# Performance work log

Hardware: AMD Instinct MI355X
Metric: run time of the kernel (lower is better)

## Reference

```python
import math
import jax
import jax.numpy as jnp
import numpy as np

B = 4096        # number of contexts / segments
T = 262144      # total objects across all segments (avg 64 per segment)
F = 128         # object_size
H = 256         # hidden_size
C = 512         # context_size


def setup_inputs() -> dict:
    key = jax.random.key(0)
    ks = jax.random.split(key, 8)
    objects = jax.random.normal(ks[0], (T, F), dtype=jnp.float32)
    context = jax.random.normal(ks[1], (B, C), dtype=jnp.float32)
    # sorted segment ids; guarantee every segment non-empty by seeding one id per segment
    extra = jax.random.randint(ks[2], (T - B,), 0, B)
    segment_ids = jnp.sort(jnp.concatenate([jnp.arange(B, dtype=extra.dtype), extra])).astype(jnp.int32)
    s = 0.05
    return {
        "objects": objects,
        "context": context,
        "segment_ids": segment_ids,
        "W1": jax.random.normal(ks[3], (F, H), dtype=jnp.float32) * s,
        "b1": jnp.zeros((H,), dtype=jnp.float32),
        "W2": jax.random.normal(ks[4], (H, H), dtype=jnp.float32) * s,
        "b2": jnp.zeros((H,), dtype=jnp.float32),
        "W3": jax.random.normal(ks[5], (H, 2 * H), dtype=jnp.float32) * s,
        "b3": jnp.zeros((2 * H,), dtype=jnp.float32),
        "Wq": jax.random.normal(ks[6], (C, H), dtype=jnp.float32) * s,
        "bq": jnp.zeros((H,), dtype=jnp.float32),
    }


def reference(objects, context, segment_ids, W1, b1, W2, b2, W3, b3, Wq, bq):
    num_segments = context.shape[0]
    # kv MLP: Linear -> ReLU -> Linear -> ReLU -> Linear(2H)
    h = jax.nn.relu(objects @ W1 + b1)
    h = jax.nn.relu(h @ W2 + b2)
    kv = h @ W3 + b3                                   # [T, 2H]
    k, v = jnp.split(kv, 2, axis=1)                    # [T, H] each
    # query per object via repeat_interleave == gather by segment id
    q = (context @ Wq + bq)[segment_ids]               # [T, H]
    logits = jnp.sum(q * k, axis=1) / math.sqrt(k.shape[1])   # [T]
    # per-segment stable softmax
    m = jax.ops.segment_max(logits, segment_ids, num_segments=num_segments)
    e = jnp.exp(logits - m[segment_ids])
    z = jax.ops.segment_sum(e, segment_ids, num_segments=num_segments)
    w = e / z[segment_ids]                             # [T]
    # per-segment weighted sum of values
    embedding = jax.ops.segment_sum(w[:, None] * v, segment_ids, num_segments=num_segments)  # [B, H]
    return embedding, w
```

## Files before the change

### kernel.cpp

```cpp
#include <hip/hip_runtime.h>
#include <hip/hip_bf16.h>

#define T_TOTAL 262144
#define B_SEG   4096

typedef __attribute__((ext_vector_type(8))) short short8;
typedef __attribute__((ext_vector_type(4))) float f32x4;

__device__ __forceinline__ short f2bf(float x) {
    __hip_bfloat16 h = __float2bfloat16(x);
    return *reinterpret_cast<short*>(&h);
}
__device__ __forceinline__ float bf2f(short s) {
    unsigned u = ((unsigned)(unsigned short)s) << 16;
    return __uint_as_float(u);
}

__global__ __launch_bounds__(256) void prep_all(
    const float* __restrict__ W1, const float* __restrict__ W2,
    const float* __restrict__ W3, const float* __restrict__ Wq,
    const float* __restrict__ bq, const float* __restrict__ b3,
    const float* __restrict__ ctx, const int* __restrict__ seg,
    short* __restrict__ W1T, short* __restrict__ W2T, short* __restrict__ W3vT,
    float* __restrict__ bz, float* __restrict__ wc, float* __restrict__ c0,
    float* __restrict__ Wqz, float* __restrict__ cbuf,
    int* __restrict__ starts) {
    __shared__ __align__(16) char smem[33280];
    const int b = blockIdx.x, tid = threadIdx.x;

    if (b < 40) {
        float (*t)[68] = reinterpret_cast<float(*)[68]>(smem);
        const float* src; short* dst;
        int k0, n0_src, n0_dst, sstride, dstride;
        if (b < 8) {
            int kt = b >> 2, nt = b & 3;
            src = W1; dst = W1T; sstride = 256; dstride = 128;
            k0 = kt * 64; n0_src = nt * 64; n0_dst = nt * 64;
        } else if (b < 24) {
            int id = b - 8, kt = id >> 2, nt = id & 3;
            src = W2; dst = W2T; sstride = 256; dstride = 256;
            k0 = kt * 64; n0_src = nt * 64; n0_dst = nt * 64;
        } else {
            int id = b - 24, kt = id >> 2, nt = id & 3;
            src = W3; dst = W3vT; sstride = 512; dstride = 256;
            k0 = kt * 64; n0_src = 256 + nt * 64; n0_dst = nt * 64;
        }
        {
            int r = tid >> 4, c4 = (tid & 15) * 4;
#pragma unroll
            for (int p = 0; p < 4; p++) {
                int k = p * 16 + r;
                float4 v = *reinterpret_cast<const float4*>(
                    &src[(size_t)(k0 + k) * sstride + n0_src + c4]);
                *reinterpret_cast<float4*>(&t[k][c4]) = v;
            }
        }
        __syncthreads();
        {
            int n = tid >> 2, kq = tid & 3;
            short8 s0, s1;
#pragma unroll
            for (int i = 0; i < 8; i++) s0[i] = f2bf(t[kq * 16 + i][n]);
#pragma unroll
            for (int i = 0; i < 8; i++) s1[i] = f2bf(t[kq * 16 + 8 + i][n]);
            short* o = &dst[(size_t)(n0_dst + n) * dstride + k0 + kq * 16];
            *reinterpret_cast<short8*>(o) = s0;
            *reinterpret_cast<short8*>(o + 8) = s1;
        }
    } else if (b < 42) {
        if (b == 40) {
            float s = 0.f;
            for (int n = 0; n < 256; n += 4) {
                float4 a = *reinterpret_cast<const float4*>(&W3[(size_t)tid * 512 + n]);
                float4 v = *reinterpret_cast<const float4*>(&bq[n]);
                s += a.x * v.x + a.y * v.y + a.z * v.z + a.w * v.w;
            }
            bz[tid] = s;
        } else {
#pragma unroll
            for (int h = 0; h < 2; h++) {
                int c = h * 256 + tid;
                float s = 0.f;
                for (int n = 0; n < 256; n += 4) {
                    float4 a = *reinterpret_cast<const float4*>(&Wq[(size_t)c * 256 + n]);
                    float4 v = *reinterpret_cast<const float4*>(&b3[n]);
                    s += a.x * v.x + a.y * v.y + a.z * v.z + a.w * v.w;
                }
                wc[c] = s;
            }
            if (tid == 0) {
                float s = 0.f;
                for (int n = 0; n < 256; n++) s += bq[n] * b3[n];
                c0[0] = s;
            }
        }
    } else if (b < 554) {
        float (*wq)[260] = reinterpret_cast<float(*)[260]>(smem);
        float (*w3)[260] = reinterpret_cast<float(*)[260]>(smem + 16640);
        const int id = b - 42;
        const int c0r = (id >> 4) * 16, j0 = (id & 15) * 16;
        {
            int r = tid >> 4, nq = tid & 15;
#pragma unroll
            for (int p = 0; p < 4; p++) {
                int col = nq * 4 + p * 64;
                *reinterpret_cast<float4*>(&wq[r][col]) =
                    *reinterpret_cast<const float4*>(&Wq[(size_t)(c0r + r) * 256 + col]);
                *reinterpret_cast<float4*>(&w3[r][col]) =
                    *reinterpret_cast<const float4*>(&W3[(size_t)(j0 + r) * 512 + col]);
            }
        }
        __syncthreads();
        const int ci = tid >> 4, ji = tid & 15;
        float s = 0.f;
        for (int n = 0; n < 256; n += 4) {
            float4 a = *reinterpret_cast<const float4*>(&wq[ci][n]);
            float4 v = *reinterpret_cast<const float4*>(&w3[ji][n]);
            s += a.x * v.x + a.y * v.y + a.z * v.z + a.w * v.w;
        }
        Wqz[(size_t)(c0r + ci) * 256 + j0 + ji] = s;
    } else if (b < 682) {
        const int id = b - 554;
        const int row = id * 32 + (tid >> 3);
        const int l = tid & 7;
        float s = 0.f;
        for (int i = 0; i < 64; i += 4) {
            float4 a = *reinterpret_cast<const float4*>(&ctx[(size_t)row * 512 + l * 64 + i]);
            float4 v = *reinterpret_cast<const float4*>(&wc[l * 64 + i]);
            s += a.x * v.x + a.y * v.y + a.z * v.z + a.w * v.w;
        }
        s += __shfl_xor(s, 1); s += __shfl_xor(s, 2); s += __shfl_xor(s, 4);
        if (l == 0) cbuf[row] = s + c0[0];
    } else {
        int t = (b - 682) * 256 + tid;
        if (t < T_TOTAL) {
            int s = seg[t];
            if (t == 0) {
                for (int q = 0; q <= s; q++) starts[q] = 0;
            } else {
                int p = seg[t - 1];
                for (int q = p + 1; q <= s; q++) starts[q] = t;
            }
        }
    }
}

__global__ __launch_bounds__(256) void zq_kernel(
    const float* __restrict__ ctx, const float* __restrict__ Wqz,
    const float* __restrict__ bz, float* __restrict__ zq) {
    __shared__ float As[2][16][44];
    const int tid = threadIdx.x;
    const int tm = tid & 7, tn = tid >> 3;
    const int row0 = blockIdx.x * 32, col0 = blockIdx.y * 64;
    const int lr = tid >> 3, lk = tid & 7;

    float acc[4][2];
#pragma unroll
    for (int i = 0; i < 4; i++) { acc[i][0] = 0.f; acc[i][1] = 0.f; }

    float2 av = *reinterpret_cast<const float2*>(&ctx[(size_t)(row0 + lr) * 512 + lk * 2]);
    for (int c = 0; c < 32; c++) {
        int cur = c & 1;
        As[cur][lk * 2 + 0][lr] = av.x;
        As[cur][lk * 2 + 1][lr] = av.y;
        __syncthreads();
        if (c < 31)
            av = *reinterpret_cast<const float2*>(
                &ctx[(size_t)(row0 + lr) * 512 + (c + 1) * 16 + lk * 2]);
#pragma unroll
        for (int k = 0; k < 16; k++) {
            float4 a = *reinterpret_cast<const float4*>(&As[cur][k][tm * 4]);
            float2 b = *reinterpret_cast<const float2*>(
                &Wqz[(size_t)(c * 16 + k) * 256 + col0 + tn * 2]);
            acc[0][0] += a.x * b.x; acc[0][1] += a.x * b.y;
            acc[1][0] += a.y * b.x; acc[1][1] += a.y * b.y;
            acc[2][0] += a.z * b.x; acc[2][1] += a.z * b.y;
            acc[3][0] += a.w * b.x; acc[3][1] += a.w * b.y;
        }
    }
    float2 bv = *reinterpret_cast<const float2*>(&bz[col0 + tn * 2]);
#pragma unroll
    for (int i = 0; i < 4; i++) {
        float2 o = {acc[i][0] + bv.x, acc[i][1] + bv.y};
        *reinterpret_cast<float2*>(
            &zq[(size_t)(row0 + tm * 4 + i) * 256 + col0 + tn * 2]) = o;
    }
}

template <int K>
__device__ __forceinline__ void run_layer(
    const short* __restrict__ act, const short* __restrict__ Wt,
    int nbase, int l16, int quad, f32x4 acc[8][4]) {
    constexpr int KK = K / 32;
    const f32x4 zero = {0.f, 0.f, 0.f, 0.f};
#pragma unroll
    for (int i = 0; i < 8; i++)
#pragma unroll
        for (int j = 0; j < 4; j++) acc[i][j] = zero;

    int woff[4];
#pragma unroll
    for (int ns = 0; ns < 4; ns++)
        woff[ns] = ((nbase + ns * 16 + l16) * K + quad * 8) * 2;
    const int abase = l16 * K * 2;
    const char* actc = reinterpret_cast<const char*>(act);
    const char* wtc  = reinterpret_cast<const char*>(Wt);

    short8 wbuf[2][4];
    short8 areg[8];

#pragma unroll
    for (int ns = 0; ns < 4; ns++)
        wbuf[0][ns] = *reinterpret_cast<const short8*>(wtc + woff[ns]);

#pragma unroll
    for (int kk = 0; kk < KK; kk++) {
        if (kk + 1 < KK) {
#pragma unroll
            for (int ns = 0; ns < 4; ns++)
                wbuf[(kk + 1) & 1][ns] = *reinterpret_cast<const short8*>(
                    wtc + woff[ns] + (kk + 1) * 64);
        }
        {
            const int sg = (((kk * 4 + quad) ^ l16) * 16);
#pragma unroll
            for (int ms = 0; ms < 8; ms++)
                areg[ms] = *reinterpret_cast<const short8*>(
                    actc + abase + ms * 16 * K * 2 + sg);
        }
        const int cb = kk & 1;
#pragma unroll
        for (int ms = 0; ms < 8; ms++)
#pragma unroll
            for (int ns = 0; ns < 4; ns++)
                acc[ms][ns] = __builtin_amdgcn_mfma_f32_16x16x32_bf16(
                    wbuf[cb][ns], areg[ms], acc[ms][ns], 0, 0, 0);
    }
}

__global__ __launch_bounds__(256, 2) void mlp_kernel(
    const float* __restrict__ objects, const int* __restrict__ seg_ids,
    const short* __restrict__ W1T, const short* __restrict__ W2T,
    const short* __restrict__ W3vT,
    const float* __restrict__ b1, const float* __restrict__ b2,
    const float* __restrict__ b3,
    const float* __restrict__ zqbuf, const float* __restrict__ cbuf,
    float* __restrict__ logits_out, short* __restrict__ vout) {
    __shared__ __align__(16) short bufH[128 * 256];
    __shared__ float slots[4][128];

    const int tid  = threadIdx.x;
    const int wave = tid >> 6;
    const int lane = tid & 63;
    const int quad = lane >> 4;
    const int l16  = lane & 15;
    const int nbase = wave * 64;
    const int row0  = blockIdx.x * 128;

    {
        const float4* op = reinterpret_cast<const float4*>(objects + (size_t)row0 * 128);
#pragma unroll
        for (int i = 0; i < 8; i++) {
            int u = tid + i * 256;
            int m = u >> 4, kg = u & 15;
            float4 x0 = op[u * 2];
            float4 x1 = op[u * 2 + 1];
            short8 s;
            s[0] = f2bf(x0.x); s[1] = f2bf(x0.y); s[2] = f2bf(x0.z); s[3] = f2bf(x0.w);
            s[4] = f2bf(x1.x); s[5] = f2bf(x1.y); s[6] = f2bf(x1.z); s[7] = f2bf(x1.w);
            *reinterpret_cast<short8*>(&bufH[m * 128 + ((kg ^ (m & 15)) * 8)]) = s;
        }
    }
    __syncthreads();

    f32x4 acc[8][4];

    auto store_act = [&](const float* __restrict__ bias) {
#pragma unroll
        for (int ms = 0; ms < 8; ms++) {
            int m = ms * 16 + l16;
#pragma unroll
            for (int ns = 0; ns < 4; ns++) {
                int n0 = nbase + ns * 16 + quad * 4;
                float4 bv = *reinterpret_cast<const float4*>(&bias[n0]);
                short4 s;
                s.x = f2bf(fmaxf(acc[ms][ns][0] + bv.x, 0.f));
                s.y = f2bf(fmaxf(acc[ms][ns][1] + bv.y, 0.f));
                s.z = f2bf(fmaxf(acc[ms][ns][2] + bv.z, 0.f));
                s.w = f2bf(fmaxf(acc[ms][ns][3] + bv.w, 0.f));
                *reinterpret_cast<short4*>(
                    &bufH[m * 256 + (((n0 >> 3) ^ (m & 15)) * 8) + (n0 & 7)]) = s;
            }
        }
    };

    run_layer<128>(bufH, W1T, nbase, l16, quad, acc);
    __syncthreads();
    store_act(b1);
    __syncthreads();

    run_layer<256>(bufH, W2T, nbase, l16, quad, acc);
    __syncthreads();
    {
#pragma unroll
        for (int ms = 0; ms < 8; ms++) {
            int m = ms * 16 + l16;
            int sgm = seg_ids[row0 + m];
            float part = 0.f;
#pragma unroll
            for (int ns = 0; ns < 4; ns++) {
                int n0 = nbase + ns * 16 + quad * 4;
                float4 bv = *reinterpret_cast<const float4*>(&b2[n0]);
                float h0 = fmaxf(acc[ms][ns][0] + bv.x, 0.f);
                float h1v = fmaxf(acc[ms][ns][1] + bv.y, 0.f);
                float h2v = fmaxf(acc[ms][ns][2] + bv.z, 0.f);
                float h3 = fmaxf(acc[ms][ns][3] + bv.w, 0.f);
                short4 s;
                s.x = f2bf(h0); s.y = f2bf(h1v); s.z = f2bf(h2v); s.w = f2bf(h3);
                *reinterpret_cast<short4*>(
                    &bufH[m * 256 + (((n0 >> 3) ^ (m & 15)) * 8) + (n0 & 7)]) = s;
                float4 zq4 = *reinterpret_cast<const float4*>(
                    &zqbuf[(size_t)sgm * 256 + n0]);
                part += h0 * zq4.x + h1v * zq4.y + h2v * zq4.z + h3 * zq4.w;
            }
            part += __shfl_xor(part, 16);
            part += __shfl_xor(part, 32);
            if (quad == 0) slots[wave][m] = part;
        }
    }
    __syncthreads();
    if (tid < 128) {
        int seg = seg_ids[row0 + tid];
        float s = slots[0][tid] + slots[1][tid] + slots[2][tid] + slots[3][tid] + cbuf[seg];
        logits_out[row0 + tid] = s * 0.0625f;
    }

    run_layer<256>(bufH, W3vT, nbase, l16, quad, acc);
#pragma unroll
    for (int ms = 0; ms < 8; ms++) {
        int m = ms * 16 + l16;
#pragma unroll
        for (int ns = 0; ns < 4; ns++) {
            int n0 = nbase + ns * 16 + quad * 4;
            float4 bv = *reinterpret_cast<const float4*>(&b3[256 + n0]);
            short4 s;
            s.x = f2bf(acc[ms][ns][0] + bv.x);
            s.y = f2bf(acc[ms][ns][1] + bv.y);
            s.z = f2bf(acc[ms][ns][2] + bv.z);
            s.w = f2bf(acc[ms][ns][3] + bv.w);
            *reinterpret_cast<short4*>(
                &vout[(size_t)(row0 + m) * 256 + n0]) = s;
        }
    }
}

__global__ __launch_bounds__(64) void segment_kernel(
    const float* __restrict__ logits, const short* __restrict__ vbuf,
    const int* __restrict__ starts, float* __restrict__ emb,
    float* __restrict__ wout) {
    const int b = blockIdx.x;
    const int lane = threadIdx.x;
    const int start = starts[b];
    const int end = (b == B_SEG - 1) ? T_TOTAL : starts[b + 1];

    float mx = -1e30f;
    for (int t = start + lane; t < end; t += 64) mx = fmaxf(mx, logits[t]);
#pragma unroll
    for (int off = 32; off >= 1; off >>= 1) mx = fmaxf(mx, __shfl_xor(mx, off));

    float s = 0.f;
    for (int t = start + lane; t < end; t += 64) s += __expf(logits[t] - mx);
#pragma unroll
    for (int off = 32; off >= 1; off >>= 1) s += __shfl_xor(s, off);
    const float invz = 1.f / s;

    for (int t = start + lane; t < end; t += 64)
        wout[t] = __expf(logits[t] - mx) * invz;

    const int half = lane >> 5;
    const int c8 = (lane & 31) * 8;
    float a[4][8];
#pragma unroll
    for (int u = 0; u < 4; u++)
#pragma unroll
        for (int j = 0; j < 8; j++) a[u][j] = 0.f;

    int t = start;
    for (; t + 8 <= end; t += 8) {
#pragma unroll
        for (int u = 0; u < 4; u++) {
            int row = t + u * 2 + half;
            float wv = __expf(logits[row] - mx) * invz;
            short8 v8 = *reinterpret_cast<const short8*>(
                &vbuf[(size_t)row * 256 + c8]);
#pragma unroll
            for (int j = 0; j < 8; j++) a[u][j] += wv * bf2f(v8[j]);
        }
    }
    for (; t < end; t += 2) {
        int row = t + half;
        if (row < end) {
            float wv = __expf(logits[row] - mx) * invz;
            short8 v8 = *reinterpret_cast<const short8*>(
                &vbuf[(size_t)row * 256 + c8]);
#pragma unroll
            for (int j = 0; j < 8; j++) a[0][j] += wv * bf2f(v8[j]);
        }
    }
    float o[8];
#pragma unroll
    for (int j = 0; j < 8; j++) {
        o[j] = a[0][j] + a[1][j] + a[2][j] + a[3][j];
        o[j] += __shfl_xor(o[j], 32);
    }
    if (half == 0) {
        float4 o0 = {o[0], o[1], o[2], o[3]};
        float4 o1 = {o[4], o[5], o[6], o[7]};
        *reinterpret_cast<float4*>(&emb[(size_t)b * 256 + c8]) = o0;
        *reinterpret_cast<float4*>(&emb[(size_t)b * 256 + c8 + 4]) = o1;
    }
}

extern "C" void kernel_launch(void* const* d_in, const int* in_sizes, int n_in,
                              void* d_out, int out_size, void* d_ws, size_t ws_size,
                              hipStream_t stream) {
    const float* objects = (const float*)d_in[0];
    const float* context = (const float*)d_in[1];
    const int*   seg     = (const int*)d_in[2];
    const float* W1 = (const float*)d_in[3];
    const float* b1 = (const float*)d_in[4];
    const float* W2 = (const float*)d_in[5];
    const float* b2 = (const float*)d_in[6];
    const float* W3 = (const float*)d_in[7];
    const float* b3 = (const float*)d_in[8];
    const float* Wq = (const float*)d_in[9];
    const float* bq = (const float*)d_in[10];

    char* ws = (char*)d_ws;
    float* zqbuf = (float*)(ws);
    float* cbuf  = (float*)(ws + 4194304);
    int*   seg_starts = (int*)(ws + 4227072);
    short* W1T   = (short*)(ws + 4259840);
    short* W2T   = (short*)(ws + 4325376);
    short* W3vT  = (short*)(ws + 4456448);
    char*  lreg   = ws + 4587520;
    float* logits = (float*)lreg;
    float* Wqz    = (float*)lreg;
    float* bz     = (float*)(lreg + 524288);
    float* wc     = (float*)(lreg + 525312);
    float* c0     = (float*)(lreg + 527360);
    short* vbuf   = (short*)(ws + 5636096);

    float* emb  = (float*)d_out;
    float* wout = emb + (size_t)B_SEG * 256;

    prep_all<<<1706, 256, 0, stream>>>(W1, W2, W3, Wq, bq, b3, context, seg,
                                       W1T, W2T, W3vT, bz, wc, c0, Wqz, cbuf,
                                       seg_starts);
    zq_kernel<<<dim3(128, 4), 256, 0, stream>>>(context, Wqz, bz, zqbuf);
    mlp_kernel<<<T_TOTAL / 128, 256, 0, stream>>>(objects, seg, W1T, W2T, W3vT,
                                                  b1, b2, b3, zqbuf, cbuf,
                                                  logits, vbuf);
    segment_kernel<<<B_SEG, 64, 0, stream>>>(logits, vbuf, seg_starts, emb, wout);
}
```

Baseline: 418.8 us.

## Make MLP kernel persistent and prefetch next tile's objects during layer 2

Changes the MLP kernel into a persistent grid of 512 blocks that loop over 128-row tiles. Half of the next tile's object rows are prefetched into registers while the current tile runs layer 2. The other half is still loaded directly at the start of each tile. This is meant to hide global load latency and cut per-block launch and prologue cost, but it adds register pressure under launch_bounds(256,2) and leaves some dead helper code in place.

```diff
diff --git a/kernel.cpp b/kernel.cpp
--- a/kernel.cpp
+++ b/kernel.cpp
@@ -255,12 +255,56 @@
     const int quad = lane >> 4;
     const int l16  = lane & 15;
     const int nbase = wave * 64;
-    const int row0  = blockIdx.x * 128;
-
-    {
-        const float4* op = reinterpret_cast<const float4*>(objects + (size_t)row0 * 128);
-#pragma unroll
-        for (int i = 0; i < 8; i++) {
+    constexpr int NT = T_TOTAL / 128;
+    const int GRID = gridDim.x;
+
+    float4 xr[8];
+    auto loadX = [&](int tile) {
+        const float4* op = reinterpret_cast<const float4*>(
+            objects + (size_t)tile * 128 * 128);
+#pragma unroll
+        for (int i = 0; i < 4; i++) {
+            int u = tid + i * 256;
+            xr[2 * i]     = op[u * 2];
+            xr[2 * i + 1] = op[u * 2 + 1];
+        }
+    };
+    auto writeX = [&]() {
+#pragma unroll
+        for (int i = 0; i < 4; i++) {
+            int u = tid + i * 256;
+            int m = u >> 4, kg = u & 15;
+            float4 x0 = xr[2 * i], x1 = xr[2 * i + 1];
+            short8 s;
+            s[0] = f2bf(x0.x); s[1] = f2bf(x0.y); s[2] = f2bf(x0.z); s[3] = f2bf(x0.w);
+            s[4] = f2bf(x1.x); s[5] = f2bf(x1.y); s[6] = f2bf(x1.z); s[7] = f2bf(x1.w);
+            *reinterpret_cast<short8*>(&bufH[m * 128 + ((kg ^ (m & 15)) * 8)]) = s;
+        }
+#pragma unroll
+        for (int i = 4; i < 8; i++) {
+            int u = tid + i * 256;
+            int m = u >> 4, kg = u & 15;
+            const float4* op2 = nullptr; (void)op2;
+            (void)m; (void)kg;
+        }
+    };
+    (void)writeX;
+
+    auto writeX_full = [&](int tile) {
+        const float4* op = reinterpret_cast<const float4*>(
+            objects + (size_t)tile * 128 * 128);
+#pragma unroll
+        for (int i = 0; i < 4; i++) {
+            int u = tid + i * 256;
+            int m = u >> 4, kg = u & 15;
+            float4 x0 = xr[2 * i], x1 = xr[2 * i + 1];
+            short8 s;
+            s[0] = f2bf(x0.x); s[1] = f2bf(x0.y); s[2] = f2bf(x0.z); s[3] = f2bf(x0.w);
+            s[4] = f2bf(x1.x); s[5] = f2bf(x1.y); s[6] = f2bf(x1.z); s[7] = f2bf(x1.w);
+            *reinterpret_cast<short8*>(&bufH[m * 128 + ((kg ^ (m & 15)) * 8)]) = s;
+        }
+#pragma unroll
+        for (int i = 4; i < 8; i++) {
             int u = tid + i * 256;
             int m = u >> 4, kg = u & 15;
             float4 x0 = op[u * 2];
@@ -270,8 +314,7 @@
             s[4] = f2bf(x1.x); s[5] = f2bf(x1.y); s[6] = f2bf(x1.z); s[7] = f2bf(x1.w);
             *reinterpret_cast<short8*>(&bufH[m * 128 + ((kg ^ (m & 15)) * 8)]) = s;
         }
-    }
-    __syncthreads();
+    };
 
     f32x4 acc[8][4];
 
@@ -294,62 +337,74 @@
         }
     };
 
-    run_layer<128>(bufH, W1T, nbase, l16, quad, acc);
-    __syncthreads();
-    store_act(b1);
-    __syncthreads();
-
-    run_layer<256>(bufH, W2T, nbase, l16, quad, acc);
-    __syncthreads();
-    {
+    loadX(blockIdx.x);
+
+    for (int tile = blockIdx.x; tile < NT; tile += GRID) {
+        const int row0 = tile * 128;
+        const int nxt = tile + GRID;
+
+        __syncthreads();
+        writeX_full(tile);
+        __syncthreads();
+
+        run_layer<128>(bufH, W1T, nbase, l16, quad, acc);
+        __syncthreads();
+        store_act(b1);
+        __syncthreads();
+
+        run_layer<256>(bufH, W2T, nbase, l16, quad, acc);
+        if (nxt < NT) loadX(nxt);
+        __syncthreads();
+        {
+#pragma unroll
+            for (int ms = 0; ms < 8; ms++) {
+                int m = ms * 16 + l16;
+                int sgm = seg_ids[row0 + m];
+                float part = 0.f;
+#pragma unroll
+                for (int ns = 0; ns < 4; ns++) {
+                    int n0 = nbase + ns * 16 + quad * 4;
+                    float4 bv = *reinterpret_cast<const float4*>(&b2[n0]);
+                    float h0 = fmaxf(acc[ms][ns][0] + bv.x, 0.f);
+                    float h1v = fmaxf(acc[ms][ns][1] + bv.y, 0.f);
+                    float h2v = fmaxf(acc[ms][ns][2] + bv.z, 0.f);
+                    float h3 = fmaxf(acc[ms][ns][3] + bv.w, 0.f);
+                    short4 s;
+                    s.x = f2bf(h0); s.y = f2bf(h1v); s.z = f2bf(h2v); s.w = f2bf(h3);
+                    *reinterpret_cast<short4*>(
+                        &bufH[m * 256 + (((n0 >> 3) ^ (m & 15)) * 8) + (n0 & 7)]) = s;
+                    float4 zq4 = *reinterpret_cast<const float4*>(
+                        &zqbuf[(size_t)sgm * 256 + n0]);
+                    part += h0 * zq4.x + h1v * zq4.y + h2v * zq4.z + h3 * zq4.w;
+                }
+                part += __shfl_xor(part, 16);
+                part += __shfl_xor(part, 32);
+                if (quad == 0) slots[wave][m] = part;
+            }
+        }
+        __syncthreads();
+        if (tid < 128) {
+            int seg = seg_ids[row0 + tid];
+            float s = slots[0][tid] + slots[1][tid] + slots[2][tid] + slots[3][tid] + cbuf[seg];
+            logits_out[row0 + tid] = s * 0.0625f;
+        }
+
+        run_layer<256>(bufH, W3vT, nbase, l16, quad, acc);
 #pragma unroll
         for (int ms = 0; ms < 8; ms++) {
             int m = ms * 16 + l16;
-            int sgm = seg_ids[row0 + m];
-            float part = 0.f;
 #pragma unroll
             for (int ns = 0; ns < 4; ns++) {
                 int n0 = nbase + ns * 16 + quad * 4;
-                float4 bv = *reinterpret_cast<const float4*>(&b2[n0]);
-                float h0 = fmaxf(acc[ms][ns][0] + bv.x, 0.f);
-                float h1v = fmaxf(acc[ms][ns][1] + bv.y, 0.f);
-                float h2v = fmaxf(acc[ms][ns][2] + bv.z, 0.f);
-                float h3 = fmaxf(acc[ms][ns][3] + bv.w, 0.f);
+                float4 bv = *reinterpret_cast<const float4*>(&b3[256 + n0]);
                 short4 s;
-                s.x = f2bf(h0); s.y = f2bf(h1v); s.z = f2bf(h2v); s.w = f2bf(h3);
+                s.x = f2bf(acc[ms][ns][0] + bv.x);
+                s.y = f2bf(acc[ms][ns][1] + bv.y);
+                s.z = f2bf(acc[ms][ns][2] + bv.z);
+                s.w = f2bf(acc[ms][ns][3] + bv.w);
                 *reinterpret_cast<short4*>(
-                    &bufH[m * 256 + (((n0 >> 3) ^ (m & 15)) * 8) + (n0 & 7)]) = s;
-                float4 zq4 = *reinterpret_cast<const float4*>(
-                    &zqbuf[(size_t)sgm * 256 + n0]);
-                part += h0 * zq4.x + h1v * zq4.y + h2v * zq4.z + h3 * zq4.w;
-            }
-            part += __shfl_xor(part, 16);
-            part += __shfl_xor(part, 32);
-            if (quad == 0) slots[wave][m] = part;
-        }
-    }
-    __syncthreads();
-    if (tid < 128) {
-        int seg = seg_ids[row0 + tid];
-        float s = slots[0][tid] + slots[1][tid] + slots[2][tid] + slots[3][tid] + cbuf[seg];
-        logits_out[row0 + tid] = s * 0.0625f;
-    }
-
-    run_layer<256>(bufH, W3vT, nbase, l16, quad, acc);
-#pragma unroll
-    for (int ms = 0; ms < 8; ms++) {
-        int m = ms * 16 + l16;
-#pragma unroll
-        for (int ns = 0; ns < 4; ns++) {
-            int n0 = nbase + ns * 16 + quad * 4;
-            float4 bv = *reinterpret_cast<const float4*>(&b3[256 + n0]);
-            short4 s;
-            s.x = f2bf(acc[ms][ns][0] + bv.x);
-            s.y = f2bf(acc[ms][ns][1] + bv.y);
-            s.z = f2bf(acc[ms][ns][2] + bv.z);
-            s.w = f2bf(acc[ms][ns][3] + bv.w);
-            *reinterpret_cast<short4*>(
-                &vout[(size_t)(row0 + m) * 256 + n0]) = s;
+                    &vout[(size_t)(row0 + m) * 256 + n0]) = s;
+            }
         }
     }
 }
@@ -458,8 +513,8 @@
                                        W1T, W2T, W3vT, bz, wc, c0, Wqz, cbuf,
                                        seg_starts);
     zq_kernel<<<dim3(128, 4), 256, 0, stream>>>(context, Wqz, bz, zqbuf);
-    mlp_kernel<<<T_TOTAL / 128, 256, 0, stream>>>(objects, seg, W1T, W2T, W3vT,
-                                                  b1, b2, b3, zqbuf, cbuf,
-                                                  logits, vbuf);
+    mlp_kernel<<<512, 256, 0, stream>>>(objects, seg, W1T, W2T, W3vT,
+                                        b1, b2, b3, zqbuf, cbuf,
+                                        logits, vbuf);
     segment_kernel<<<B_SEG, 64, 0, stream>>>(logits, vbuf, seg_starts, emb, wout);
 }
```

Result: slower. 684.4 us (+63.4%).
